# Performance work log

Measured on AMD Instinct MI355X. Metric: run time of the kernel, lower is better.

## Reference

```python
import jax, jax.numpy as jnp
import numpy as np

N_GROUP = 8
TOPK_GROUP = 4
TOP_K = 8
ROUTED_SCALING_FACTOR = 2.5
RENORMALIZE = True


def setup_inputs() -> dict:
    key = jax.random.key(0)
    k1, k2 = jax.random.split(key)
    num_tokens, n_experts = 131072, 256
    router_logits = jax.random.normal(k1, (num_tokens, n_experts), dtype=jnp.float32)
    e_score_correction_bias = jax.random.normal(k2, (n_experts,), dtype=jnp.float32) * 0.1
    return {"router_logits": router_logits,
            "e_score_correction_bias": e_score_correction_bias}


def reference(router_logits, e_score_correction_bias):
    T, E = router_logits.shape
    per_group = E // N_GROUP  # 32 experts per group

    # sigmoid scoring + bias correction (bias used for selection only)
    scores = jax.nn.sigmoid(router_logits)                      # [T, E]
    scores_for_choice = scores + e_score_correction_bias[None, :]

    # group score = sum of top-2 corrected scores within each group
    grouped = scores_for_choice.reshape(T, N_GROUP, per_group)  # [T, G, E/G]
    top2_vals, _ = jax.lax.top_k(grouped, 2)                    # [T, G, 2]
    group_scores = top2_vals.sum(axis=-1)                       # [T, G]

    # pick topk_group groups, build expert-level mask
    _, group_idx = jax.lax.top_k(group_scores, TOPK_GROUP)      # [T, topk_group]
    group_mask = jnp.zeros((T, N_GROUP), dtype=jnp.bool_)
    group_mask = group_mask.at[jnp.arange(T)[:, None], group_idx].set(True)
    score_mask = jnp.repeat(group_mask, per_group, axis=1)      # [T, E]

    # mask non-selected groups, then global top-k over remaining experts
    masked_scores = jnp.where(score_mask, scores_for_choice, 0.0)
    _, topk_ids = jax.lax.top_k(masked_scores, TOP_K)           # [T, top_k]

    # gather UNcorrected sigmoid scores as weights
    topk_weights = jnp.take_along_axis(scores, topk_ids, axis=1)  # [T, top_k]
    if RENORMALIZE:
        topk_weights = topk_weights / (topk_weights.sum(axis=-1, keepdims=True) + 1e-20)
    topk_weights = topk_weights * ROUTED_SCALING_FACTOR
    return topk_weights, topk_ids
```

## Files before the change

### kernel.cpp

```cpp
#include <hip/hip_runtime.h>
#include <math.h>

#define THREADS 256
#define TPB 32
#define NEXP 256
#define EPS_S 2.0e-6f
#define EPS_G 4.0e-6f

__device__ __forceinline__ float fsigmoid(float x) {
    float e = __expf(-x);
    return __fdividef(1.0f, 1.0f + e);
}

__device__ __forceinline__ double dsigmoid(float xf) {
    xf = fminf(fmaxf(xf, -500.0f), 500.0f);
    double x = (double)xf;
    double t = x * -1.4426950408889634074;
    double n = floor(t + 0.5);
    int ni = (int)n;
    double u = (t - n) * 0.69314718055994530942;
    double pp = 2.08767569878680990e-9;
    pp = fma(pp, u, 2.50521083854417188e-8);
    pp = fma(pp, u, 2.75573192239858907e-7);
    pp = fma(pp, u, 2.75573192239858883e-6);
    pp = fma(pp, u, 2.48015873015873016e-5);
    pp = fma(pp, u, 1.98412698412698413e-4);
    pp = fma(pp, u, 1.38888888888888889e-3);
    pp = fma(pp, u, 8.33333333333333333e-3);
    pp = fma(pp, u, 4.16666666666666667e-2);
    pp = fma(pp, u, 1.66666666666666667e-1);
    pp = fma(pp, u, 0.5);
    pp = fma(pp, u, 1.0);
    pp = fma(pp, u, 1.0);
    double sc = __longlong_as_double((long long)(1023 + ni) << 52);
    double e = pp * sc;
    double w = 1.0 + e;
    double y = (double)__fdividef(1.0f, (float)w);
    y = fma(y, fma(-w, y, 1.0), y);
    y = fma(y, fma(-w, y, 1.0), y);
    return y;
}

#define MINS(cc, ee) do {                                                \
    float _c=(cc); int _e=(ee);                                          \
    if (_c > m8) {                                                       \
        bool _b0=_c>m0,_b1=_c>m1,_b2=_c>m2,_b3=_c>m3,_b4=_c>m4,          \
             _b5=_c>m5,_b6=_c>m6,_b7=_c>m7;                              \
        m8=_b7?m7:_c;           n8=_b7?n7:_e;                            \
        m7=_b6?m6:(_b7?_c:m7);  n7=_b6?n6:(_b7?_e:n7);                   \
        m6=_b5?m5:(_b6?_c:m6);  n6=_b5?n5:(_b6?_e:n6);                   \
        m5=_b4?m4:(_b5?_c:m5);  n5=_b4?n4:(_b5?_e:n5);                   \
        m4=_b3?m3:(_b4?_c:m4);  n4=_b3?n3:(_b4?_e:n4);                   \
        m3=_b2?m2:(_b3?_c:m3);  n3=_b2?n2:(_b3?_e:n3);                   \
        m2=_b1?m1:(_b2?_c:m2);  n2=_b1?n1:(_b2?_e:n2);                   \
        m1=_b0?m0:(_b1?_c:m1);  n1=_b0?n0:(_b1?_e:n1);                   \
        m0=_b0?_c:m0;           n0=_b0?_e:n0;                            \
    } } while (0)

#define DINS(cc, ee) do {                                                \
    double _d=(cc); int _e=(ee);                                         \
    if (_d > s7) {                                                       \
        bool _b0=_d>s0,_b1=_d>s1,_b2=_d>s2,_b3=_d>s3,_b4=_d>s4,          \
             _b5=_d>s5,_b6=_d>s6;                                        \
        s7=_b6?s6:_d;           c7=_b6?c6:_e;                            \
        s6=_b5?s5:(_b6?_d:s6);  c6=_b5?c5:(_b6?_e:c6);                   \
        s5=_b4?s4:(_b5?_d:s5);  c5=_b4?c4:(_b5?_e:c5);                   \
        s4=_b3?s3:(_b4?_d:s4);  c4=_b3?c3:(_b4?_e:c4);                   \
        s3=_b2?s2:(_b3?_d:s3);  c3=_b2?c2:(_b3?_e:c3);                   \
        s2=_b1?s1:(_b2?_d:s2);  c2=_b1?c1:(_b2?_e:c2);                   \
        s1=_b0?s0:(_b1?_d:s1);  c1=_b0?c0:(_b1?_e:c1);                   \
        s0=_b0?_d:s0;           c0=_b0?_e:c0;                            \
    } } while (0)

#define TOMAX(av, ai, bv, bi) do {                                       \
    bool _g = ((bv) > (av)) || (((bv) == (av)) && ((bi) < (ai)));        \
    (av) = _g ? (bv) : (av); (ai) = _g ? (bi) : (ai);                    \
} while (0)

#define TOCE(av, ai, bv, bi) do {                                        \
    bool _s = ((bv) > (av)) || (((bv) == (av)) && ((bi) < (ai)));        \
    float _tv = (av); int _ti = (ai);                                    \
    (av) = _s ? (bv) : (av); (ai) = _s ? (bi) : (ai);                    \
    (bv) = _s ? _tv : (bv); (bi) = _s ? _ti : (bi);                      \
} while (0)

#define XMERGE_B(d) do {                                                 \
    float q0=__shfl_xor(m0,d,64), q1=__shfl_xor(m1,d,64),                \
          q2=__shfl_xor(m2,d,64), q3=__shfl_xor(m3,d,64),                \
          q4=__shfl_xor(m4,d,64), q5=__shfl_xor(m5,d,64),                \
          q6=__shfl_xor(m6,d,64), q7=__shfl_xor(m7,d,64),                \
          q8=__shfl_xor(m8,d,64);                                        \
    int   r0=__shfl_xor(n0,d,64), r1=__shfl_xor(n1,d,64),                \
          r2=__shfl_xor(n2,d,64), r3=__shfl_xor(n3,d,64),                \
          r4=__shfl_xor(n4,d,64), r5=__shfl_xor(n5,d,64),                \
          r6=__shfl_xor(n6,d,64), r7=__shfl_xor(n7,d,64),                \
          r8=__shfl_xor(n8,d,64);                                        \
    TOMAX(m0,n0,q8,r8); TOMAX(m1,n1,q7,r7); TOMAX(m2,n2,q6,r6);          \
    TOMAX(m3,n3,q5,r5); TOMAX(m4,n4,q4,r4); TOMAX(m5,n5,q3,r3);          \
    TOMAX(m6,n6,q2,r2); TOMAX(m7,n7,q1,r1); TOMAX(m8,n8,q0,r0);          \
    TOCE(m0,n0,m8,n8);                                                   \
    TOCE(m1,n1,m5,n5); TOCE(m2,n2,m6,n6); TOCE(m3,n3,m7,n7); TOCE(m4,n4,m8,n8); \
    TOCE(m1,n1,m3,n3); TOCE(m2,n2,m4,n4); TOCE(m5,n5,m7,n7); TOCE(m6,n6,m8,n8); \
    TOCE(m1,n1,m2,n2); TOCE(m3,n3,m4,n4); TOCE(m5,n5,m6,n6); TOCE(m7,n7,m8,n8); \
} while (0)

__device__ __forceinline__ float4 shfl4(float4 v, int src) {
    float4 r;
    r.x = __shfl(v.x, src, 64);
    r.y = __shfl(v.y, src, 64);
    r.z = __shfl(v.z, src, 64);
    r.w = __shfl(v.w, src, 64);
    return r;
}

__global__ __launch_bounds__(THREADS, 6)
void noauxtc_router_kernel(const float* __restrict__ logits,
                           const float* __restrict__ bias,
                           float* __restrict__ out,
                           int T)
{
    __shared__ __align__(16) float bias_sh[NEXP];

    const int tid   = threadIdx.x;
    const int h     = tid & 7;
    const int p     = tid >> 3;
    const int tok0  = blockIdx.x * TPB;
    const int token = tok0 + p;
    const int lane  = tid & 63;
    const int base  = lane & 56;

    const float4* lg4 = (const float4*)logits;
    float4 st[8];
    #pragma unroll
    for (int k = 0; k < 8; ++k)
        st[k] = lg4[(size_t)token * 64 + h * 8 + k];

    bias_sh[tid] = bias[tid];
    __syncthreads();

    const float4* bias4 = (const float4*)bias_sh;

    float g1 = -3e38f, g2 = -3e38f;
    #pragma unroll
    for (int q = 0; q < 8; ++q) {
        float4 bb = bias4[h * 8 + q];
        float4 c;
        c.x = fsigmoid(st[q].x) + bb.x;
        c.y = fsigmoid(st[q].y) + bb.y;
        c.z = fsigmoid(st[q].z) + bb.z;
        c.w = fsigmoid(st[q].w) + bb.w;
        st[q] = c;
        float h1 = fmaxf(c.x, c.y), l1 = fminf(c.x, c.y);
        float h2 = fmaxf(c.z, c.w), l2 = fminf(c.z, c.w);
        float t1 = fmaxf(h1, h2);
        float t2 = fmaxf(fminf(h1, h2), fmaxf(l1, l2));
        g2 = fmaxf(fminf(g1, t1), fmaxf(g2, t2));
        g1 = fmaxf(g1, t1);
    }
    float gs = g1 + g2;

    float gsv[8];
    #pragma unroll
    for (int g = 0; g < 8; ++g) gsv[g] = __shfl(gs, base + g, 64);

    int selmask = 0; float val4 = 0.f, val5 = 0.f;
    #pragma unroll
    for (int a = 0; a < 8; ++a) {
        int rk = 0;
        #pragma unroll
        for (int b = 0; b < 8; ++b) {
            if (b == a) continue;
            bool beat = (b < a) ? (gsv[b] >= gsv[a]) : (gsv[b] > gsv[a]);
            rk += beat ? 1 : 0;
        }
        selmask |= (rk < 4) ? (1 << a) : 0;
        val4 = (rk == 3) ? gsv[a] : val4;
        val5 = (rk == 4) ? gsv[a] : val5;
    }

    if (__builtin_expect(val4 - val5 < EPS_G, 0)) {
        double a1 = -1e300, a2 = -1e300;
        const float* lgp = logits + (size_t)token * 256 + h * 32;
        #pragma unroll 1
        for (int k = 0; k < 32; ++k) {
            double c = dsigmoid(lgp[k]) + (double)bias_sh[h * 32 + k];
            a2 = fmax(a2, fmin(a1, c)); a1 = fmax(a1, c);
        }
        double gdo = a1 + a2;
        double gd[8];
        #pragma unroll
        for (int g = 0; g < 8; ++g) gd[g] = __shfl(gdo, base + g, 64);
        int sm = 0;
        #pragma unroll
        for (int a = 0; a < 8; ++a) {
            int rk = 0;
            #pragma unroll
            for (int b = 0; b < 8; ++b) {
                if (b == a) continue;
                bool beat = (b < a) ? (gd[b] >= gd[a]) : (gd[b] > gd[a]);
                rk += beat ? 1 : 0;
            }
            sm |= (rk < 4) ? (1 << a) : 0;
        }
        selmask = sm;
    }

    const int want = h >> 1;
    int g = 0, cnt = 0;
    #pragma unroll
    for (int a = 0; a < 8; ++a) {
        bool s = (selmask >> a) & 1;
        g = (s && (cnt == want)) ? a : g;
        cnt += s ? 1 : 0;
    }
    const int hf  = h & 1;
    const int src = base + g;

    float4 ga[4];
    #pragma unroll
    for (int j = 0; j < 4; ++j) {
        float4 t0 = shfl4(st[j],     src);
        float4 t1 = shfl4(st[j + 4], src);
        ga[j] = hf ? t1 : t0;
    }

    float m0=-3e38f,m1=-3e38f,m2=-3e38f,m3=-3e38f,m4=-3e38f,
          m5=-3e38f,m6=-3e38f,m7=-3e38f,m8=-3e38f;
    int n0=0,n1=0,n2=0,n3=0,n4=0,n5=0,n6=0,n7=0,n8=0;
    const int ebase = g * 32 + hf * 16;
    #pragma unroll
    for (int j = 0; j < 4; ++j) {
        int eb = ebase + j * 4;
        MINS(ga[j].x, eb+0); MINS(ga[j].y, eb+1);
        MINS(ga[j].z, eb+2); MINS(ga[j].w, eb+3);
    }

    XMERGE_B(1);
    XMERGE_B(2);
    XMERGE_B(4);

    float w0 = m0 - bias_sh[n0], w1 = m1 - bias_sh[n1], w2 = m2 - bias_sh[n2],
          w3 = m3 - bias_sh[n3], w4 = m4 - bias_sh[n4], w5 = m5 - bias_sh[n5],
          w6 = m6 - bias_sh[n6], w7 = m7 - bias_sh[n7];
    int o0=n0,o1=n1,o2=n2,o3=n3,o4=n4,o5=n5,o6=n6,o7=n7;

    bool flagB = (h == 0) &&
                 (((m0-m1)<EPS_S)|((m1-m2)<EPS_S)|((m2-m3)<EPS_S)|((m3-m4)<EPS_S)|
                  ((m4-m5)<EPS_S)|((m5-m6)<EPS_S)|((m6-m7)<EPS_S)|((m7-m8)<EPS_S));
    if (__builtin_expect(flagB, 0)) {
        double s0=-1e300,s1=-1e300,s2=-1e300,s3=-1e300,
               s4=-1e300,s5=-1e300,s6=-1e300,s7=-1e300;
        int c0=0,c1=0,c2=0,c3=0,c4=0,c5=0,c6=0,c7=0;
        int ci[9] = {n0,n1,n2,n3,n4,n5,n6,n7,n8};
        const float* lgt = logits + (size_t)token * 256;
        #pragma unroll 1
        for (int k = 0; k < 9; ++k) {
            int e = ci[k];
            double cs = dsigmoid(lgt[e]) + (double)bias_sh[e];
            DINS(cs, e);
        }
        w0=(float)(s0-(double)bias_sh[c0]); o0=c0;
        w1=(float)(s1-(double)bias_sh[c1]); o1=c1;
        w2=(float)(s2-(double)bias_sh[c2]); o2=c2;
        w3=(float)(s3-(double)bias_sh[c3]); o3=c3;
        w4=(float)(s4-(double)bias_sh[c4]); o4=c4;
        w5=(float)(s5-(double)bias_sh[c5]); o5=c5;
        w6=(float)(s6-(double)bias_sh[c6]); o6=c6;
        w7=(float)(s7-(double)bias_sh[c7]); o7=c7;
    }

    if (h == 0) {
        float sum = ((w0+w1)+(w2+w3)) + ((w4+w5)+(w6+w7));
        float scl = 2.5f / (sum + 1e-20f);
        float4 oa, ob;
        oa.x=w0*scl; oa.y=w1*scl; oa.z=w2*scl; oa.w=w3*scl;
        ob.x=w4*scl; ob.y=w5*scl; ob.z=w6*scl; ob.w=w7*scl;
        *(float4*)(out + (size_t)token*8)     = oa;
        *(float4*)(out + (size_t)token*8 + 4) = ob;
        float* oid = out + (size_t)T*8;
        float4 ia, ib;
        ia.x=(float)o0; ia.y=(float)o1; ia.z=(float)o2; ia.w=(float)o3;
        ib.x=(float)o4; ib.y=(float)o5; ib.z=(float)o6; ib.w=(float)o7;
        *(float4*)(oid + (size_t)token*8)     = ia;
        *(float4*)(oid + (size_t)token*8 + 4) = ib;
    }
}

extern "C" void kernel_launch(void* const* d_in, const int* in_sizes, int n_in,
                              void* d_out, int out_size, void* d_ws, size_t ws_size,
                              hipStream_t stream) {
    const float* logits = (const float*)d_in[0];
    const float* bias   = (const float*)d_in[1];
    float* out = (float*)d_out;
    int T = in_sizes[0] / NEXP;
    int nblocks = T / TPB;
    noauxtc_router_kernel<<<nblocks, THREADS, 0, stream>>>(logits, bias, out, T);
}
```

Measured before the change: 206.4 us.

## Pack quantized score and expert index into uint keys for sort-based top-9 selection

Replaces the float-value plus int-index insertion top-9 with 32-bit keys that hold a quantized corrected score in the high bits and an inverted expert index in the low byte. Each thread sorts two 8-element halves with branch-free sorting networks, then merges them, and the cross-lane merges shuffle one register per slot instead of two. This roughly halves shuffle traffic, drops the tie-break index compares and removes divergent insertion branches. The near-tie check now uses quantized key differences to decide when to fall back to the double-precision path. Launch bounds also drop from 6 to 4 blocks per SM, which allows more registers per thread at the cost of occupancy.

```diff
diff --git a/kernel.cpp b/kernel.cpp
--- a/kernel.cpp
+++ b/kernel.cpp
@@ -4,8 +4,8 @@
 #define THREADS 256
 #define TPB 32
 #define NEXP 256
-#define EPS_S 2.0e-6f
 #define EPS_G 4.0e-6f
+#define Q_EPS 9u
 
 __device__ __forceinline__ float fsigmoid(float x) {
     float e = __expf(-x);
@@ -41,22 +41,6 @@
     return y;
 }
 
-#define MINS(cc, ee) do {                                                \
-    float _c=(cc); int _e=(ee);                                          \
-    if (_c > m8) {                                                       \
-        bool _b0=_c>m0,_b1=_c>m1,_b2=_c>m2,_b3=_c>m3,_b4=_c>m4,          \
-             _b5=_c>m5,_b6=_c>m6,_b7=_c>m7;                              \
-        m8=_b7?m7:_c;           n8=_b7?n7:_e;                            \
-        m7=_b6?m6:(_b7?_c:m7);  n7=_b6?n6:(_b7?_e:n7);                   \
-        m6=_b5?m5:(_b6?_c:m6);  n6=_b5?n5:(_b6?_e:n6);                   \
-        m5=_b4?m4:(_b5?_c:m5);  n5=_b4?n4:(_b5?_e:n5);                   \
-        m4=_b3?m3:(_b4?_c:m4);  n4=_b3?n3:(_b4?_e:n4);                   \
-        m3=_b2?m2:(_b3?_c:m3);  n3=_b2?n2:(_b3?_e:n3);                   \
-        m2=_b1?m1:(_b2?_c:m2);  n2=_b1?n1:(_b2?_e:n2);                   \
-        m1=_b0?m0:(_b1?_c:m1);  n1=_b0?n0:(_b1?_e:n1);                   \
-        m0=_b0?_c:m0;           n0=_b0?_e:n0;                            \
-    } } while (0)
-
 #define DINS(cc, ee) do {                                                \
     double _d=(cc); int _e=(ee);                                         \
     if (_d > s7) {                                                       \
@@ -72,36 +56,46 @@
         s0=_b0?_d:s0;           c0=_b0?_e:c0;                            \
     } } while (0)
 
-#define TOMAX(av, ai, bv, bi) do {                                       \
-    bool _g = ((bv) > (av)) || (((bv) == (av)) && ((bi) < (ai)));        \
-    (av) = _g ? (bv) : (av); (ai) = _g ? (bi) : (ai);                    \
+__device__ __forceinline__ unsigned pack_key(float c, unsigned idflip) {
+    unsigned q = (unsigned)fmaf(c, 4194304.0f, 2097152.0f);
+    return (q << 8) + idflip;
+}
+
+#define CEU(a, b) do {                                                   \
+    unsigned _x=(a), _y=(b);                                             \
+    (a) = _x>_y ? _x : _y; (b) = _x>_y ? _y : _x;                        \
 } while (0)
-
-#define TOCE(av, ai, bv, bi) do {                                        \
-    bool _s = ((bv) > (av)) || (((bv) == (av)) && ((bi) < (ai)));        \
-    float _tv = (av); int _ti = (ai);                                    \
-    (av) = _s ? (bv) : (av); (ai) = _s ? (bi) : (ai);                    \
-    (bv) = _s ? _tv : (bv); (bi) = _s ? _ti : (bi);                      \
+#define VMU(a, b) do { (a) = (a)>(b) ? (a) : (b); } while (0)
+
+#define SORT8U(v0,v1,v2,v3,v4,v5,v6,v7) do {                             \
+    CEU(v0,v1); CEU(v2,v3); CEU(v4,v5); CEU(v6,v7);                      \
+    CEU(v0,v2); CEU(v1,v3); CEU(v4,v6); CEU(v5,v7);                      \
+    CEU(v1,v2); CEU(v5,v6);                                              \
+    CEU(v0,v4); CEU(v1,v5); CEU(v2,v6); CEU(v3,v7);                      \
+    CEU(v2,v4); CEU(v3,v5);                                              \
+    CEU(v1,v2); CEU(v3,v4); CEU(v5,v6);                                  \
 } while (0)
 
-#define XMERGE_B(d) do {                                                 \
-    float q0=__shfl_xor(m0,d,64), q1=__shfl_xor(m1,d,64),                \
-          q2=__shfl_xor(m2,d,64), q3=__shfl_xor(m3,d,64),                \
-          q4=__shfl_xor(m4,d,64), q5=__shfl_xor(m5,d,64),                \
-          q6=__shfl_xor(m6,d,64), q7=__shfl_xor(m7,d,64),                \
-          q8=__shfl_xor(m8,d,64);                                        \
-    int   r0=__shfl_xor(n0,d,64), r1=__shfl_xor(n1,d,64),                \
-          r2=__shfl_xor(n2,d,64), r3=__shfl_xor(n3,d,64),                \
-          r4=__shfl_xor(n4,d,64), r5=__shfl_xor(n5,d,64),                \
-          r6=__shfl_xor(n6,d,64), r7=__shfl_xor(n7,d,64),                \
-          r8=__shfl_xor(n8,d,64);                                        \
-    TOMAX(m0,n0,q8,r8); TOMAX(m1,n1,q7,r7); TOMAX(m2,n2,q6,r6);          \
-    TOMAX(m3,n3,q5,r5); TOMAX(m4,n4,q4,r4); TOMAX(m5,n5,q3,r3);          \
-    TOMAX(m6,n6,q2,r2); TOMAX(m7,n7,q1,r1); TOMAX(m8,n8,q0,r0);          \
-    TOCE(m0,n0,m8,n8);                                                   \
-    TOCE(m1,n1,m5,n5); TOCE(m2,n2,m6,n6); TOCE(m3,n3,m7,n7); TOCE(m4,n4,m8,n8); \
-    TOCE(m1,n1,m3,n3); TOCE(m2,n2,m4,n4); TOCE(m5,n5,m7,n7); TOCE(m6,n6,m8,n8); \
-    TOCE(m1,n1,m2,n2); TOCE(m3,n3,m4,n4); TOCE(m5,n5,m6,n6); TOCE(m7,n7,m8,n8); \
+#define CLEAN9U do {                                                     \
+    CEU(m0,m8);                                                          \
+    CEU(m1,m5); CEU(m2,m6); CEU(m3,m7); CEU(m4,m8);                      \
+    CEU(m1,m3); CEU(m2,m4); CEU(m5,m7); CEU(m6,m8);                      \
+    CEU(m1,m2); CEU(m3,m4); CEU(m5,m6); CEU(m7,m8);                      \
+} while (0)
+
+#define XMERGE_U(d) do {                                                 \
+    unsigned q0=(unsigned)__shfl_xor((int)m0,d,64),                      \
+             q1=(unsigned)__shfl_xor((int)m1,d,64),                      \
+             q2=(unsigned)__shfl_xor((int)m2,d,64),                      \
+             q3=(unsigned)__shfl_xor((int)m3,d,64),                      \
+             q4=(unsigned)__shfl_xor((int)m4,d,64),                      \
+             q5=(unsigned)__shfl_xor((int)m5,d,64),                      \
+             q6=(unsigned)__shfl_xor((int)m6,d,64),                      \
+             q7=(unsigned)__shfl_xor((int)m7,d,64),                      \
+             q8=(unsigned)__shfl_xor((int)m8,d,64);                      \
+    VMU(m0,q8); VMU(m1,q7); VMU(m2,q6); VMU(m3,q5); VMU(m4,q4);          \
+    VMU(m5,q3); VMU(m6,q2); VMU(m7,q1); VMU(m8,q0);                      \
+    CLEAN9U;                                                             \
 } while (0)
 
 __device__ __forceinline__ float4 shfl4(float4 v, int src) {
@@ -113,7 +107,7 @@
     return r;
 }
 
-__global__ __launch_bounds__(THREADS, 6)
+__global__ __launch_bounds__(THREADS, 4)
 void noauxtc_router_kernel(const float* __restrict__ logits,
                            const float* __restrict__ bias,
                            float* __restrict__ out,
@@ -224,29 +218,49 @@
         ga[j] = hf ? t1 : t0;
     }
 
-    float m0=-3e38f,m1=-3e38f,m2=-3e38f,m3=-3e38f,m4=-3e38f,
-          m5=-3e38f,m6=-3e38f,m7=-3e38f,m8=-3e38f;
-    int n0=0,n1=0,n2=0,n3=0,n4=0,n5=0,n6=0,n7=0,n8=0;
     const int ebase = g * 32 + hf * 16;
-    #pragma unroll
-    for (int j = 0; j < 4; ++j) {
-        int eb = ebase + j * 4;
-        MINS(ga[j].x, eb+0); MINS(ga[j].y, eb+1);
-        MINS(ga[j].z, eb+2); MINS(ga[j].w, eb+3);
-    }
-
-    XMERGE_B(1);
-    XMERGE_B(2);
-    XMERGE_B(4);
-
-    float w0 = m0 - bias_sh[n0], w1 = m1 - bias_sh[n1], w2 = m2 - bias_sh[n2],
-          w3 = m3 - bias_sh[n3], w4 = m4 - bias_sh[n4], w5 = m5 - bias_sh[n5],
-          w6 = m6 - bias_sh[n6], w7 = m7 - bias_sh[n7];
+    const unsigned idf = 255u - (unsigned)ebase;
+
+    unsigned k0=pack_key(ga[0].x, idf-0),  k1=pack_key(ga[0].y, idf-1),
+             k2=pack_key(ga[0].z, idf-2),  k3=pack_key(ga[0].w, idf-3),
+             k4=pack_key(ga[1].x, idf-4),  k5=pack_key(ga[1].y, idf-5),
+             k6=pack_key(ga[1].z, idf-6),  k7=pack_key(ga[1].w, idf-7);
+    unsigned l0=pack_key(ga[2].x, idf-8),  l1=pack_key(ga[2].y, idf-9),
+             l2=pack_key(ga[2].z, idf-10), l3=pack_key(ga[2].w, idf-11),
+             l4=pack_key(ga[3].x, idf-12), l5=pack_key(ga[3].y, idf-13),
+             l6=pack_key(ga[3].z, idf-14), l7=pack_key(ga[3].w, idf-15);
+
+    SORT8U(k0,k1,k2,k3,k4,k5,k6,k7);
+    SORT8U(l0,l1,l2,l3,l4,l5,l6,l7);
+
+    unsigned m0=k0, m1=k1, m2=k2, m3=k3, m4=k4, m5=k5, m6=k6, m7=k7, m8=0u;
+    VMU(m1,l7); VMU(m2,l6); VMU(m3,l5); VMU(m4,l4);
+    VMU(m5,l3); VMU(m6,l2); VMU(m7,l1); VMU(m8,l0);
+    CLEAN9U;
+
+    XMERGE_U(1);
+    XMERGE_U(2);
+    XMERGE_U(4);
+
+    unsigned q0=m0>>8, q1=m1>>8, q2=m2>>8, q3=m3>>8, q4=m4>>8,
+             q5=m5>>8, q6=m6>>8, q7=m7>>8, q8=m8>>8;
+    int n0=255-(int)(m0&255u), n1=255-(int)(m1&255u), n2=255-(int)(m2&255u),
+        n3=255-(int)(m3&255u), n4=255-(int)(m4&255u), n5=255-(int)(m5&255u),
+        n6=255-(int)(m6&255u), n7=255-(int)(m7&255u), n8=255-(int)(m8&255u);
+
+    const float QS = 2.384185791015625e-7f;
+    float v0=(float)q0*QS-0.5f, v1=(float)q1*QS-0.5f, v2=(float)q2*QS-0.5f,
+          v3=(float)q3*QS-0.5f, v4=(float)q4*QS-0.5f, v5=(float)q5*QS-0.5f,
+          v6=(float)q6*QS-0.5f, v7=(float)q7*QS-0.5f;
+
+    float w0 = v0 - bias_sh[n0], w1 = v1 - bias_sh[n1], w2 = v2 - bias_sh[n2],
+          w3 = v3 - bias_sh[n3], w4 = v4 - bias_sh[n4], w5 = v5 - bias_sh[n5],
+          w6 = v6 - bias_sh[n6], w7 = v7 - bias_sh[n7];
     int o0=n0,o1=n1,o2=n2,o3=n3,o4=n4,o5=n5,o6=n6,o7=n7;
 
     bool flagB = (h == 0) &&
-                 (((m0-m1)<EPS_S)|((m1-m2)<EPS_S)|((m2-m3)<EPS_S)|((m3-m4)<EPS_S)|
-                  ((m4-m5)<EPS_S)|((m5-m6)<EPS_S)|((m6-m7)<EPS_S)|((m7-m8)<EPS_S));
+                 ((q0-q1<Q_EPS)|(q1-q2<Q_EPS)|(q2-q3<Q_EPS)|(q3-q4<Q_EPS)|
+                  (q4-q5<Q_EPS)|(q5-q6<Q_EPS)|(q6-q7<Q_EPS)|(q7-q8<Q_EPS));
     if (__builtin_expect(flagB, 0)) {
         double s0=-1e300,s1=-1e300,s2=-1e300,s3=-1e300,
                s4=-1e300,s5=-1e300,s6=-1e300,s7=-1e300;
```

Result: faster. 198.0 us (-4.1%).
